# Optimization experiments

Hardware: AMD Instinct MI355X
Metric: run time of the kernel (lower is better)

Reference implementation:

```python
import jax, jax.numpy as jnp
import numpy as np
from jax import lax

N = 1000        # num_nodes
IN = 32         # in_features
H = 128         # hidden
M = 128         # message_size
DEG = 16        # regular degree
P = 2           # num_predictions
OUT = 10        # out_features
NUM_STARTS = 64


def setup_inputs() -> dict:
    key = jax.random.key(0)
    ks = jax.random.split(key, 12)
    s = 0.1
    return {
        "xa": jax.random.normal(ks[0], (N, IN), jnp.float32),
        "first_message": jax.random.normal(ks[1], (N, M), jnp.float32),
        "neighbors": jax.random.randint(ks[2], (N, DEG), 0, N, dtype=jnp.int32),
        "num_starts": NUM_STARTS,
        "enc_w": jax.random.normal(ks[3], (IN, H), jnp.float32) * s,
        "enc_b": jnp.zeros((H,), jnp.float32),
        "ns_w": jax.random.normal(ks[4], (H + M, H), jnp.float32) * s,
        "ns_b": jnp.zeros((H,), jnp.float32),
        "nm_w": jax.random.normal(ks[5], (H + M, M), jnp.float32) * s,
        "nm_b": jnp.zeros((M,), jnp.float32),
        "act_w": jax.random.normal(ks[6], (H + M, 1), jnp.float32) * s,
        "act_b": jnp.zeros((1,), jnp.float32),
        "dec_w": jax.random.normal(ks[7], (P, H, OUT), jnp.float32) * s,
        "dec_b": jnp.zeros((P, OUT), jnp.float32),
    }


def reference(xa, first_message, neighbors, num_starts,
              enc_w, enc_b, ns_w, ns_b, nm_w, nm_b, act_w, act_b, dec_w, dec_b):
    n = xa.shape[0]
    deg = neighbors.shape[1]
    m = first_message.shape[1]
    max_msgs = 10 * n                      # messages < num_nodes * 10 cap
    cap = num_starts + max_msgs * deg      # max queue size (static)

    feats0 = xa @ enc_w + enc_b            # encoder, latest state per node
    qn = jnp.zeros((cap,), jnp.int32).at[:num_starts].set(
        jnp.arange(num_starts, dtype=jnp.int32))
    qm = jnp.zeros((cap, m), feats0.dtype).at[:num_starts].set(
        first_message[:num_starts])

    carry = (jnp.int32(0), jnp.int32(num_starts), qn, qm,
             feats0, jnp.zeros_like(feats0), jnp.zeros((n,), feats0.dtype))

    def step(c, _):
        head, tail, qn, qm, feats, final, tact = c
        active = head < tail                          # queue nonempty
        node = qn[head]
        msg = lax.dynamic_slice(qm, (head, 0), (1, m))[0]
        ta = tact[node]
        proc = active & (ta <= 1.0 - 1e-7)            # ACT halting check
        f = feats[node]
        x = jnp.concatenate([f, msg])                 # [H+M]
        cand = jax.nn.sigmoid(x @ act_w + act_b)[0]
        new_act = jnp.where(ta + cand > 1.0, 1.0 - ta, cand)
        ns = jax.nn.relu(x @ ns_w + ns_b)             # new state [H]
        nm_ = jnp.concatenate([ns, msg]) @ nm_w + nm_b  # new message [M]
        # enqueue deg neighbor messages (gated write)
        old_n = lax.dynamic_slice(qn, (tail,), (deg,))
        old_m = lax.dynamic_slice(qm, (tail, 0), (deg, m))
        qn = lax.dynamic_update_slice(
            qn, jnp.where(proc, neighbors[node], old_n), (tail,))
        qm = lax.dynamic_update_slice(
            qm, jnp.where(proc, jnp.broadcast_to(nm_, (deg, m)), old_m), (tail, 0))
        feats = feats.at[node].set(jnp.where(proc, ns, f))
        final = final.at[node].add(jnp.where(proc, ns * new_act, 0.0))
        tact = tact.at[node].add(jnp.where(proc, new_act, 0.0))
        head = head + active.astype(jnp.int32)
        tail = tail + proc.astype(jnp.int32) * deg
        return (head, tail, qn, qm, feats, final, tact), None

    (_, _, _, _, _, final, _), _ = lax.scan(step, carry, None, length=max_msgs)

    g = jnp.sum(final, axis=0, keepdims=True)          # graph_class readout [1,H]
    logits = jnp.einsum('nh,pho->pno', g, dec_w) + dec_b[:, None, :]
    return jax.nn.log_softmax(logits, axis=-1)         # [P, 1, OUT]
```

## Files before the change

### kernel.cpp

```cpp
#include <hip/hip_runtime.h>
#include <math.h>

#define NN 1000
#define INF_ 32
#define H 128
#define M 128
#define DEG 16
#define PP 2
#define OUTF 10
#define MAXM (10 * NN)
#define QCAP (MAXM + DEG)
#define NSLOT (MAXM + 128)
#define NT 512
#define WQ (2 * NT)
#define WROW 264
#define NROW 136

typedef _Float16 half8 __attribute__((ext_vector_type(8)));
typedef float floatx4 __attribute__((ext_vector_type(4)));

__device__ __forceinline__ void bar_lds() {
    asm volatile("s_waitcnt lgkmcnt(0)\n\ts_barrier" ::: "memory");
}

__global__ __launch_bounds__(128)
void init_kernel(const float* __restrict__ xa, const float* __restrict__ fm,
                 const float* __restrict__ enc_w, const float* __restrict__ enc_b,
                 const int* __restrict__ nstart_p,
                 _Float16* __restrict__ feats_h, float* __restrict__ finalv,
                 _Float16* __restrict__ nmbuf_h) {
    int b = blockIdx.x, t = threadIdx.x;
    float acc = enc_b[t];
    const float* xr = xa + b * INF_;
#pragma unroll
    for (int k = 0; k < INF_; ++k) acc += xr[k] * enc_w[k * H + t];
    feats_h[b * H + t] = (_Float16)acc;
    finalv[b * H + t] = 0.0f;
    if (b < nstart_p[0]) nmbuf_h[(size_t)b * M + t] = (_Float16)fm[b * M + t];
}

__global__ __launch_bounds__(256)
void pack_kernel(const float* __restrict__ ns_w, const float* __restrict__ nm_w,
                 _Float16* __restrict__ wnsB, _Float16* __restrict__ wnmB) {
    const int idx = blockIdx.x * 256 + threadIdx.x;
    if (idx >= 128 * WROW) return;
    const int n = idx / WROW, k = idx % WROW;
    wnsB[idx] = (k < 256) ? (_Float16)ns_w[k * H + n] : (_Float16)0.0f;
    wnmB[idx] = (k < 256) ? (_Float16)nm_w[k * M + n] : (_Float16)0.0f;
}

__global__ __launch_bounds__(NT, 1)
void seq_kernel(const int* __restrict__ neighbors,
                const float* __restrict__ ns_b, const float* __restrict__ nm_b,
                const float* __restrict__ act_w, const float* __restrict__ act_b,
                const float* __restrict__ dec_w, const float* __restrict__ dec_b,
                const int* __restrict__ nstart_p,
                const _Float16* __restrict__ wnsB, const _Float16* __restrict__ wnmB,
                _Float16* __restrict__ feats_h, float* __restrict__ finalv,
                _Float16* __restrict__ nmbuf_h, unsigned int* __restrict__ qpack_unused,
                float* __restrict__ out) {
    __shared__ __align__(16) _Float16 s_Xh[2][32 * WROW];
    __shared__ __align__(16) _Float16 s_NSh[2][32 * NROW];
    __shared__ unsigned int s_q[QCAP];
    __shared__ unsigned short s_nb[NN * DEG];
    __shared__ float s_tact[NN];
    __shared__ int   s_mark[NN];
    __shared__ float s_actw[H + M];
    __shared__ float s_nsb[H];
    __shared__ float s_nmb[M];
    __shared__ float s_rna[2][32];
    __shared__ unsigned short s_rns[2 * WQ];
    __shared__ unsigned int  s_enq[WQ];
    __shared__ unsigned char s_flag[NT];
    __shared__ int s_wc[8], s_wd[8];
    __shared__ int s_cnt;

    unsigned short* const s_rnode = s_rns;
    short* s_order = (short*)s_mark;
    float* s_g  = (float*)(s_mark + 512);
    float* s_lg = (float*)(s_mark + 512 + 128);

    const int t = threadIdx.x;
    const int lane = t & 63, wid = t >> 6;
    const int quad = lane >> 4, lm = lane & 15;
    const int q4 = quad << 2;
    const int colw = (wid << 4) + lm;
    const int sg = t & 31;
    const int r16 = t >> 5, c8 = t & 31;
    const int rowc = t >> 4, c16 = t & 15;
    const int nstart = nstart_p[0];
    const int rsoff = (c8 < 16) ? 0 : WQ;
    const _Float16* const gsrc = (c8 < 16) ? (feats_h + c8 * 8)
                                           : (nmbuf_h + (c8 - 16) * 8);

    half8 wbn[8], wbm[8];
#pragma unroll
    for (int c = 0; c < 8; ++c) {
        wbn[c] = *(const half8*)(wnsB + (size_t)colw * WROW + (c << 5) + (quad << 3));
        wbm[c] = *(const half8*)(wnmB + (size_t)colw * WROW + (c << 5) + (quad << 3));
    }

    for (int i = t; i < NN; i += NT) { s_tact[i] = 0.0f; s_mark[i] = 0x7fffffff; }
    for (int i = t; i < nstart; i += NT) s_q[i] = (unsigned)i | ((unsigned)i << 16);
    for (int i = t; i < NN * DEG; i += NT) s_nb[i] = (unsigned short)neighbors[i];
    if (t < H + M) s_actw[t] = act_w[t];
    if (t < H) { s_nsb[t] = ns_b[t]; s_nmb[t] = nm_b[t]; }
    const float actb = act_b[0];
    __syncthreads();
    const float nsb_c = s_nsb[colw];
    const float nmb_c = s_nmb[colw];
    float aw[8];
#pragma unroll
    for (int j = 0; j < 8; ++j) aw[j] = s_actw[sg * 8 + j];

    auto gate = [&](uint4 v) -> float {
        const half8 hv = *(const half8*)&v;
        float p = 0.0f;
#pragma unroll
        for (int j = 0; j < 8; ++j) p += (float)hv[j] * aw[j];
#pragma unroll
        for (int off = 16; off > 0; off >>= 1) p += __shfl_down(p, off, 32);
        return p;
    };

    int head = 0, tail = nstart, gbase = nstart;
    for (;;) {
        const int lim = min(tail, MAXM);
        if (head >= lim) break;
        const int W = min(WQ, lim - head);

        int nodeA = 0, slotA = 0; bool remA = false;
        int nodeB = 0, slotB = 0; bool remB = false;
        if (t < W) {
            const unsigned v = s_q[head + t];
            nodeA = (int)(v & 0xffffu);
            slotA = (int)(v >> 16);
            remA = (s_tact[nodeA] <= 1.0f - 1e-7f);
        }
        if (NT + t < W) {
            const unsigned v = s_q[head + NT + t];
            nodeB = (int)(v & 0xffffu);
            slotB = (int)(v >> 16);
            remB = (s_tact[nodeB] <= 1.0f - 1e-7f);
        }
        s_flag[t] = 0;
        s_mark[t] = 0x7fffffff;
        bar_lds();

        int base = 0;
        for (;;) {
            const bool rem2a = remA && (s_tact[nodeA] <= 1.0f - 1e-7f);
            const bool rem2b = remB && (s_tact[nodeB] <= 1.0f - 1e-7f);
            if (rem2a) atomicMin(&s_mark[nodeA], t);
            if (rem2b) atomicMin(&s_mark[nodeB], NT + t);
            if (t == 0) s_cnt = 0;
            asm volatile("s_waitcnt vmcnt(0)" ::: "memory");
            bar_lds();
            const bool winA = rem2a && (s_mark[nodeA] == t);
            const bool winB = rem2b && (s_mark[nodeB] == NT + t);
            const unsigned long long ma = __ballot(winA);
            const unsigned long long mb = __ballot(winB);
            const int ca = __popcll(ma), cb = __popcll(mb);
            int wbase = 0;
            if (lane == 0 && (ca + cb)) wbase = atomicAdd(&s_cnt, ca + cb);
            wbase = __shfl(wbase, 0, 64);
            const unsigned long long below = (1ull << lane) - 1ull;
            if (winA) {
                const int wrank = wbase + __popcll(ma & below);
                s_rns[wrank] = (unsigned short)nodeA;
                s_rns[WQ + wrank] = (unsigned short)slotA;
                s_enq[t] = (unsigned)nodeA | ((unsigned)(gbase + base + wrank) << 16);
                s_flag[t] |= 1;
            }
            if (winB) {
                const int wrank = wbase + ca + __popcll(mb & below);
                s_rns[wrank] = (unsigned short)nodeB;
                s_rns[WQ + wrank] = (unsigned short)slotB;
                s_enq[NT + t] = (unsigned)nodeB | ((unsigned)(gbase + base + wrank) << 16);
                s_flag[t] |= 2;
            }
            remA = rem2a && !winA;
            remB = rem2b && !winB;
            bar_lds();
            if (rem2a) s_mark[nodeA] = 0x7fffffff;
            if (rem2b) s_mark[nodeB] = 0x7fffffff;
            const int Pr = s_cnt;
            if (Pr == 0) break;

            uint4 pxL = *(const uint4*)(gsrc + (size_t)s_rns[rsoff + min(r16, Pr - 1)] * 128);
            uint4 pxU = *(const uint4*)(gsrc + (size_t)s_rns[rsoff + min(16 + r16, Pr - 1)] * 128);
            *(uint4*)(s_Xh[0] + r16 * WROW + (c8 << 3)) = pxL;
            *(uint4*)(s_Xh[0] + (16 + r16) * WROW + (c8 << 3)) = pxU;
            float zredCL = gate(pxL);
            float zredCU = gate(pxU);
            if (Pr > 32) {
                pxL = *(const uint4*)(gsrc + (size_t)s_rns[rsoff + min(32 + r16, Pr - 1)] * 128);
                pxU = *(const uint4*)(gsrc + (size_t)s_rns[rsoff + min(48 + r16, Pr - 1)] * 128);
            }
            bar_lds();

            floatx4 accmPL = {0, 0, 0, 0}, accmPU = {0, 0, 0, 0};
            float nsvPL[4] = {0, 0, 0, 0}, nsvPU[4] = {0, 0, 0, 0};
            int PcPL = 0, PcPU = 0, sbP = 0, c0P = 0;

            auto phase2 = [&](int pb) {
                {
                    const _Float16* nrow = s_NSh[pb] + lm * NROW + (quad << 3);
#pragma unroll
                    for (int c = 0; c < 4; ++c)
                        accmPL = __builtin_amdgcn_mfma_f32_16x16x32_f16(
                            *(const half8*)(nrow + (c << 5)), wbm[c], accmPL, 0, 0, 0);
                }
                {
                    const _Float16* nrow = s_NSh[pb] + (16 + lm) * NROW + (quad << 3);
#pragma unroll
                    for (int c = 0; c < 4; ++c)
                        accmPU = __builtin_amdgcn_mfma_f32_16x16x32_f16(
                            *(const half8*)(nrow + (c << 5)), wbm[c], accmPU, 0, 0, 0);
                }
                float naL[4], naU[4];
                int nrL[4], nrU[4];
#pragma unroll
                for (int i = 0; i < 4; ++i) {
                    naL[i] = s_rna[pb][q4 + i];
                    naU[i] = s_rna[pb][16 + q4 + i];
                    nrL[i] = (int)s_rnode[c0P + q4 + i];
                    nrU[i] = (int)s_rnode[c0P + 16 + q4 + i];
                }
                if (PcPU == 16) {
#pragma unroll
                    for (int i = 0; i < 4; ++i) {
                        nmbuf_h[(size_t)(sbP + q4 + i) * M + colw] =
                            (_Float16)(accmPL[i] + nmb_c);
                        nmbuf_h[(size_t)(sbP + 16 + q4 + i) * M + colw] =
                            (_Float16)(accmPU[i] + nmb_c);
                    }
#pragma unroll
                    for (int i = 0; i < 4; ++i) {
                        atomicAdd(finalv + (size_t)nrL[i] * H + colw, nsvPL[i] * naL[i]);
                        atomicAdd(finalv + (size_t)nrU[i] * H + colw, nsvPU[i] * naU[i]);
                    }
                } else {
#pragma unroll
                    for (int i = 0; i < 4; ++i) {
                        const int r = q4 + i;
                        if (r < PcPL) {
                            nmbuf_h[(size_t)(sbP + r) * M + colw] =
                                (_Float16)(accmPL[i] + nmb_c);
                            atomicAdd(finalv + (size_t)nrL[i] * H + colw,
                                      nsvPL[i] * naL[i]);
                        }
                        if (r < PcPU) {
                            nmbuf_h[(size_t)(sbP + 16 + r) * M + colw] =
                                (_Float16)(accmPU[i] + nmb_c);
                            atomicAdd(finalv + (size_t)nrU[i] * H + colw,
                                      nsvPU[i] * naU[i]);
                        }
                    }
                }
                if (rowc < PcPL || (unsigned)(rowc - 16) < (unsigned)PcPU) {
                    const int nrr = (int)s_rnode[c0P + rowc];
                    const uint4 v = *(const uint4*)(s_NSh[pb] + rowc * NROW + (c16 << 3));
                    *(uint4*)(feats_h + (size_t)nrr * H + (c16 << 3)) = v;
                }
            };

            for (int c0 = 0; c0 < Pr; c0 += 32) {
                const int k = c0 >> 5;
                const int cur = k & 1, nxt = cur ^ 1;
                const int remn = Pr - c0;
                const int PcL = (remn >= 16) ? 16 : remn;
                const int PcU = (remn >= 32) ? 16 : (remn > 16 ? remn - 16 : 0);
                const bool hasnext = remn > 32;
                float zredNL = 0.0f, zredNU = 0.0f;
                if (hasnext) {
                    *(uint4*)(s_Xh[nxt] + r16 * WROW + (c8 << 3)) = pxL;
                    *(uint4*)(s_Xh[nxt] + (16 + r16) * WROW + (c8 << 3)) = pxU;
                    zredNL = gate(pxL);
                    zredNU = gate(pxU);
                }
                if (remn > 64) {
                    pxL = *(const uint4*)(gsrc + (size_t)s_rns[rsoff + min(c0 + 64 + r16, Pr - 1)] * 128);
                    pxU = *(const uint4*)(gsrc + (size_t)s_rns[rsoff + min(c0 + 80 + r16, Pr - 1)] * 128);
                }
                if (c0 > 0) phase2(nxt);
                if (sg == 0) {
                    if (r16 < PcL) {
                        const float z = zredCL + actb;
                        const float cnd = 1.0f / (1.0f + expf(-z));
                        const int nr = (int)s_rnode[c0 + r16];
                        const float ta = s_tact[nr];
                        const float na = (ta + cnd > 1.0f) ? (1.0f - ta) : cnd;
                        s_rna[cur][r16] = na;
                        s_tact[nr] = ta + na;
                    }
                    if (r16 < PcU) {
                        const float z = zredCU + actb;
                        const float cnd = 1.0f / (1.0f + expf(-z));
                        const int nr = (int)s_rnode[c0 + 16 + r16];
                        const float ta = s_tact[nr];
                        const float na = (ta + cnd > 1.0f) ? (1.0f - ta) : cnd;
                        s_rna[cur][16 + r16] = na;
                        s_tact[nr] = ta + na;
                    }
                }
                floatx4 accmL, accmU;
                float nsvL[4], nsvU[4];
                {
                    floatx4 accn = {0, 0, 0, 0}, accm = {0, 0, 0, 0};
                    const _Float16* xrow = s_Xh[cur] + lm * WROW + (quad << 3);
                    half8 a[8];
#pragma unroll
                    for (int c = 0; c < 8; ++c) a[c] = *(const half8*)(xrow + (c << 5));
#pragma unroll
                    for (int c = 0; c < 8; ++c)
                        accn = __builtin_amdgcn_mfma_f32_16x16x32_f16(a[c], wbn[c], accn, 0, 0, 0);
#pragma unroll
                    for (int c = 4; c < 8; ++c)
                        accm = __builtin_amdgcn_mfma_f32_16x16x32_f16(a[c], wbm[c], accm, 0, 0, 0);
#pragma unroll
                    for (int i = 0; i < 4; ++i) {
                        nsvL[i] = fmaxf(accn[i] + nsb_c, 0.0f);
                        s_NSh[cur][(q4 + i) * NROW + colw] = (_Float16)nsvL[i];
                    }
                    accmL = accm;
                }
                {
                    floatx4 accn = {0, 0, 0, 0}, accm = {0, 0, 0, 0};
                    const _Float16* xrow = s_Xh[cur] + (16 + lm) * WROW + (quad << 3);
                    half8 a[8];
#pragma unroll
                    for (int c = 0; c < 8; ++c) a[c] = *(const half8*)(xrow + (c << 5));
#pragma unroll
                    for (int c = 0; c < 8; ++c)
                        accn = __builtin_amdgcn_mfma_f32_16x16x32_f16(a[c], wbn[c], accn, 0, 0, 0);
#pragma unroll
                    for (int c = 4; c < 8; ++c)
                        accm = __builtin_amdgcn_mfma_f32_16x16x32_f16(a[c], wbm[c], accm, 0, 0, 0);
#pragma unroll
                    for (int i = 0; i < 4; ++i) {
                        nsvU[i] = fmaxf(accn[i] + nsb_c, 0.0f);
                        s_NSh[cur][(16 + q4 + i) * NROW + colw] = (_Float16)nsvU[i];
                    }
                    accmU = accm;
                }
                accmPL = accmL; accmPU = accmU;
#pragma unroll
                for (int i = 0; i < 4; ++i) { nsvPL[i] = nsvL[i]; nsvPU[i] = nsvU[i]; }
                PcPL = PcL; PcPU = PcU; sbP = gbase + base + c0; c0P = c0;
                zredCL = zredNL; zredCU = zredNU;
                bar_lds();
            }
            phase2((c0P >> 5) & 1);
            base += Pr;
        }

        const bool pfa = (s_flag[t] & 1) != 0;
        const bool pfb = (s_flag[t] & 2) != 0;
        const unsigned long long mfa = __ballot(pfa);
        const unsigned long long mfb = __ballot(pfb);
        if (lane == 0) { s_wc[wid] = __popcll(mfa); s_wd[wid] = __popcll(mfb); }
        bar_lds();
        int TA = 0, TB = 0, preA = 0, preB = 0;
#pragma unroll
        for (int w = 0; w < 8; ++w) {
            TA += s_wc[w]; TB += s_wd[w];
            preA += (w < wid) ? s_wc[w] : 0;
            preB += (w < wid) ? s_wd[w] : 0;
        }
        const int T = TA + TB;
        if (T > 0) {
            const unsigned long long below = (1ull << lane) - 1ull;
            if (pfa) s_order[preA + __popcll(mfa & below)] = (short)t;
            if (pfb) s_order[TA + preB + __popcll(mfb & below)] = (short)(NT + t);
            bar_lds();
            for (int idx = t; idx < T * DEG; idx += NT) {
                const int e = (int)s_order[idx >> 4];
                const unsigned v = s_enq[e];
                const int nd = (int)(v & 0xffffu);
                const unsigned slot = v >> 16;
                const int q = tail + idx;
                if (q < QCAP)
                    s_q[q] = (unsigned)s_nb[nd * DEG + (idx & 15)] | (slot << 16);
            }
        }
        tail += DEG * T;
        gbase += T;
        head += W;
        bar_lds();
    }

    __syncthreads();

    if (t < H) {
        float g0 = 0, g1 = 0, g2 = 0, g3 = 0;
        for (int n = 0; n < NN; n += 4) {
            g0 += finalv[(n + 0) * H + t];
            g1 += finalv[(n + 1) * H + t];
            g2 += finalv[(n + 2) * H + t];
            g3 += finalv[(n + 3) * H + t];
        }
        s_g[t] = (g0 + g1) + (g2 + g3);
    }
    __syncthreads();
    if (t < PP * OUTF) {
        const int pp = t / OUTF, o = t % OUTF;
        float acc = dec_b[pp * OUTF + o];
        for (int h = 0; h < H; ++h) acc += s_g[h] * dec_w[(pp * H + h) * OUTF + o];
        s_lg[t] = acc;
    }
    __syncthreads();
    if (t < PP * OUTF) {
        const int pp = t / OUTF;
        float mx = -INFINITY;
        for (int o = 0; o < OUTF; ++o) mx = fmaxf(mx, s_lg[pp * OUTF + o]);
        float s = 0.0f;
        for (int o = 0; o < OUTF; ++o) s += expf(s_lg[pp * OUTF + o] - mx);
        out[t] = s_lg[t] - (mx + logf(s));
    }
}

extern "C" void kernel_launch(void* const* d_in, const int* in_sizes, int n_in,
                              void* d_out, int out_size, void* d_ws, size_t ws_size,
                              hipStream_t stream) {
    const float* xa        = (const float*)d_in[0];
    const float* fm        = (const float*)d_in[1];
    const int*   neighbors = (const int*)  d_in[2];
    const int*   nstart_p  = (const int*)  d_in[3];
    const float* enc_w     = (const float*)d_in[4];
    const float* enc_b     = (const float*)d_in[5];
    const float* ns_w      = (const float*)d_in[6];
    const float* ns_b      = (const float*)d_in[7];
    const float* nm_w      = (const float*)d_in[8];
    const float* nm_b      = (const float*)d_in[9];
    const float* act_w     = (const float*)d_in[10];
    const float* act_b     = (const float*)d_in[11];
    const float* dec_w     = (const float*)d_in[12];
    const float* dec_b     = (const float*)d_in[13];
    float* out = (float*)d_out;

    char* w = (char*)d_ws;
    _Float16* feats_h = (_Float16*)w;                 w += (size_t)NN * H * 2;
    float*    finalv  = (float*)w;                    w += (size_t)NN * H * 4;
    _Float16* nmbuf_h = (_Float16*)w;                 w += (size_t)NSLOT * M * 2;
    _Float16* wnsB    = (_Float16*)w;                 w += (size_t)128 * WROW * 2;
    _Float16* wnmB    = (_Float16*)w;                 w += (size_t)128 * WROW * 2;
    unsigned int* qpack = (unsigned int*)w;

    init_kernel<<<NN, 128, 0, stream>>>(xa, fm, enc_w, enc_b, nstart_p,
                                        feats_h, finalv, nmbuf_h);
    pack_kernel<<<132, 256, 0, stream>>>(ns_w, nm_w, wnsB, wnmB);
    seq_kernel<<<1, NT, 0, stream>>>(neighbors, ns_b, nm_b,
                                     act_w, act_b, dec_w, dec_b, nstart_p,
                                     wnsB, wnmB,
                                     feats_h, finalv, nmbuf_h, qpack, out);
}
```

Before: 524.8 us.

## Stage new-message outputs in LDS and skip empty upper half-tiles

Inner 32-row chunks now write new-message results to an LDS staging buffer, then copy them out to global memory one iteration later as coalesced 16-byte row stores. Before, each lane did scattered 2-byte stores. The phase2 lambda is inlined and only the tail chunk keeps the guarded partial path. The upper 16-row MFMA block and its gather are skipped when a chunk has no upper rows. The vmcnt wait is moved later so it overlaps the winner-selection work. This adds LDS usage and makes the pipelining logic more complex, with a risk to correctness in edge cases.

```diff
diff --git a/kernel.cpp b/kernel.cpp
--- a/kernel.cpp
+++ b/kernel.cpp
@@ -61,6 +61,7 @@
                 float* __restrict__ out) {
     __shared__ __align__(16) _Float16 s_Xh[2][32 * WROW];
     __shared__ __align__(16) _Float16 s_NSh[2][32 * NROW];
+    __shared__ __align__(16) _Float16 s_NMh[2][32 * NROW];
     __shared__ unsigned int s_q[QCAP];
     __shared__ unsigned short s_nb[NN * DEG];
     __shared__ float s_tact[NN];
@@ -154,7 +155,6 @@
             if (rem2a) atomicMin(&s_mark[nodeA], t);
             if (rem2b) atomicMin(&s_mark[nodeB], NT + t);
             if (t == 0) s_cnt = 0;
-            asm volatile("s_waitcnt vmcnt(0)" ::: "memory");
             bar_lds();
             const bool winA = rem2a && (s_mark[nodeA] == t);
             const bool winB = rem2b && (s_mark[nodeB] == NT + t);
@@ -181,18 +181,23 @@
             }
             remA = rem2a && !winA;
             remB = rem2b && !winB;
+            asm volatile("s_waitcnt vmcnt(0)" ::: "memory");
             bar_lds();
             if (rem2a) s_mark[nodeA] = 0x7fffffff;
             if (rem2b) s_mark[nodeB] = 0x7fffffff;
             const int Pr = s_cnt;
             if (Pr == 0) break;
+            const int sb0 = gbase + base;
 
             uint4 pxL = *(const uint4*)(gsrc + (size_t)s_rns[rsoff + min(r16, Pr - 1)] * 128);
             uint4 pxU = *(const uint4*)(gsrc + (size_t)s_rns[rsoff + min(16 + r16, Pr - 1)] * 128);
             *(uint4*)(s_Xh[0] + r16 * WROW + (c8 << 3)) = pxL;
-            *(uint4*)(s_Xh[0] + (16 + r16) * WROW + (c8 << 3)) = pxU;
             float zredCL = gate(pxL);
-            float zredCU = gate(pxU);
+            float zredCU = 0.0f;
+            if (Pr > 16) {
+                *(uint4*)(s_Xh[0] + (16 + r16) * WROW + (c8 << 3)) = pxU;
+                zredCU = gate(pxU);
+            }
             if (Pr > 32) {
                 pxL = *(const uint4*)(gsrc + (size_t)s_rns[rsoff + min(32 + r16, Pr - 1)] * 128);
                 pxU = *(const uint4*)(gsrc + (size_t)s_rns[rsoff + min(48 + r16, Pr - 1)] * 128);
@@ -201,69 +206,6 @@
 
             floatx4 accmPL = {0, 0, 0, 0}, accmPU = {0, 0, 0, 0};
             float nsvPL[4] = {0, 0, 0, 0}, nsvPU[4] = {0, 0, 0, 0};
-            int PcPL = 0, PcPU = 0, sbP = 0, c0P = 0;
-
-            auto phase2 = [&](int pb) {
-                {
-                    const _Float16* nrow = s_NSh[pb] + lm * NROW + (quad << 3);
-#pragma unroll
-                    for (int c = 0; c < 4; ++c)
-                        accmPL = __builtin_amdgcn_mfma_f32_16x16x32_f16(
-                            *(const half8*)(nrow + (c << 5)), wbm[c], accmPL, 0, 0, 0);
-                }
-                {
-                    const _Float16* nrow = s_NSh[pb] + (16 + lm) * NROW + (quad << 3);
-#pragma unroll
-                    for (int c = 0; c < 4; ++c)
-                        accmPU = __builtin_amdgcn_mfma_f32_16x16x32_f16(
-                            *(const half8*)(nrow + (c << 5)), wbm[c], accmPU, 0, 0, 0);
-                }
-                float naL[4], naU[4];
-                int nrL[4], nrU[4];
-#pragma unroll
-                for (int i = 0; i < 4; ++i) {
-                    naL[i] = s_rna[pb][q4 + i];
-                    naU[i] = s_rna[pb][16 + q4 + i];
-                    nrL[i] = (int)s_rnode[c0P + q4 + i];
-                    nrU[i] = (int)s_rnode[c0P + 16 + q4 + i];
-                }
-                if (PcPU == 16) {
-#pragma unroll
-                    for (int i = 0; i < 4; ++i) {
-                        nmbuf_h[(size_t)(sbP + q4 + i) * M + colw] =
-                            (_Float16)(accmPL[i] + nmb_c);
-                        nmbuf_h[(size_t)(sbP + 16 + q4 + i) * M + colw] =
-                            (_Float16)(accmPU[i] + nmb_c);
-                    }
-#pragma unroll
-                    for (int i = 0; i < 4; ++i) {
-                        atomicAdd(finalv + (size_t)nrL[i] * H + colw, nsvPL[i] * naL[i]);
-                        atomicAdd(finalv + (size_t)nrU[i] * H + colw, nsvPU[i] * naU[i]);
-                    }
-                } else {
-#pragma unroll
-                    for (int i = 0; i < 4; ++i) {
-                        const int r = q4 + i;
-                        if (r < PcPL) {
-                            nmbuf_h[(size_t)(sbP + r) * M + colw] =
-                                (_Float16)(accmPL[i] + nmb_c);
-                            atomicAdd(finalv + (size_t)nrL[i] * H + colw,
-                                      nsvPL[i] * naL[i]);
-                        }
-                        if (r < PcPU) {
-                            nmbuf_h[(size_t)(sbP + 16 + r) * M + colw] =
-                                (_Float16)(accmPU[i] + nmb_c);
-                            atomicAdd(finalv + (size_t)nrU[i] * H + colw,
-                                      nsvPU[i] * naU[i]);
-                        }
-                    }
-                }
-                if (rowc < PcPL || (unsigned)(rowc - 16) < (unsigned)PcPU) {
-                    const int nrr = (int)s_rnode[c0P + rowc];
-                    const uint4 v = *(const uint4*)(s_NSh[pb] + rowc * NROW + (c16 << 3));
-                    *(uint4*)(feats_h + (size_t)nrr * H + (c16 << 3)) = v;
-                }
-            };
 
             for (int c0 = 0; c0 < Pr; c0 += 32) {
                 const int k = c0 >> 5;
@@ -271,19 +213,60 @@
                 const int remn = Pr - c0;
                 const int PcL = (remn >= 16) ? 16 : remn;
                 const int PcU = (remn >= 32) ? 16 : (remn > 16 ? remn - 16 : 0);
-                const bool hasnext = remn > 32;
                 float zredNL = 0.0f, zredNU = 0.0f;
-                if (hasnext) {
+                if (remn > 32) {
                     *(uint4*)(s_Xh[nxt] + r16 * WROW + (c8 << 3)) = pxL;
-                    *(uint4*)(s_Xh[nxt] + (16 + r16) * WROW + (c8 << 3)) = pxU;
                     zredNL = gate(pxL);
-                    zredNU = gate(pxU);
+                    if (remn > 48) {
+                        *(uint4*)(s_Xh[nxt] + (16 + r16) * WROW + (c8 << 3)) = pxU;
+                        zredNU = gate(pxU);
+                    }
                 }
                 if (remn > 64) {
                     pxL = *(const uint4*)(gsrc + (size_t)s_rns[rsoff + min(c0 + 64 + r16, Pr - 1)] * 128);
                     pxU = *(const uint4*)(gsrc + (size_t)s_rns[rsoff + min(c0 + 80 + r16, Pr - 1)] * 128);
                 }
-                if (c0 > 0) phase2(nxt);
+                if (c0 >= 64) {
+                    const int sbC = sb0 + c0 - 64;
+                    const uint4 v = *(const uint4*)(s_NMh[cur] + rowc * NROW + (c16 << 3));
+                    *(uint4*)(nmbuf_h + (size_t)(sbC + rowc) * M + (c16 << 3)) = v;
+                }
+                if (c0 > 0) {
+                    const int c0F = c0 - 32;
+                    {
+                        const _Float16* nrow = s_NSh[nxt] + lm * NROW + (quad << 3);
+#pragma unroll
+                        for (int c = 0; c < 4; ++c)
+                            accmPL = __builtin_amdgcn_mfma_f32_16x16x32_f16(
+                                *(const half8*)(nrow + (c << 5)), wbm[c], accmPL, 0, 0, 0);
+                    }
+                    {
+                        const _Float16* nrow = s_NSh[nxt] + (16 + lm) * NROW + (quad << 3);
+#pragma unroll
+                        for (int c = 0; c < 4; ++c)
+                            accmPU = __builtin_amdgcn_mfma_f32_16x16x32_f16(
+                                *(const half8*)(nrow + (c << 5)), wbm[c], accmPU, 0, 0, 0);
+                    }
+#pragma unroll
+                    for (int i = 0; i < 4; ++i) {
+                        s_NMh[nxt][(q4 + i) * NROW + colw] = (_Float16)(accmPL[i] + nmb_c);
+                        s_NMh[nxt][(16 + q4 + i) * NROW + colw] = (_Float16)(accmPU[i] + nmb_c);
+                    }
+#pragma unroll
+                    for (int i = 0; i < 4; ++i) {
+                        const float naL = s_rna[nxt][q4 + i];
+                        const float naU = s_rna[nxt][16 + q4 + i];
+                        const int nrL = (int)s_rnode[c0F + q4 + i];
+                        const int nrU = (int)s_rnode[c0F + 16 + q4 + i];
+                        atomicAdd(finalv + (size_t)nrL * H + colw, nsvPL[i] * naL);
+                        atomicAdd(finalv + (size_t)nrU * H + colw, nsvPU[i] * naU);
+                    }
+                    {
+                        const int nrr = (int)s_rnode[c0F + rowc];
+                        const uint4 v = *(const uint4*)(s_NSh[nxt] + rowc * NROW + (c16 << 3));
+                        *(uint4*)(feats_h + (size_t)nrr * H + (c16 << 3)) = v;
+                    }
+                }
                 if (sg == 0) {
                     if (r16 < PcL) {
                         const float z = zredCL + actb;
@@ -304,8 +287,8 @@
                         s_tact[nr] = ta + na;
                     }
                 }
-                floatx4 accmL, accmU;
-                float nsvL[4], nsvU[4];
+                floatx4 accmL = {0, 0, 0, 0}, accmU = {0, 0, 0, 0};
+                float nsvL[4] = {0, 0, 0, 0}, nsvU[4] = {0, 0, 0, 0};
                 {
                     floatx4 accn = {0, 0, 0, 0}, accm = {0, 0, 0, 0};
                     const _Float16* xrow = s_Xh[cur] + lm * WROW + (quad << 3);
@@ -325,7 +308,7 @@
                     }
                     accmL = accm;
                 }
-                {
+                if (PcU > 0) {
                     floatx4 accn = {0, 0, 0, 0}, accm = {0, 0, 0, 0};
                     const _Float16* xrow = s_Xh[cur] + (16 + lm) * WROW + (quad << 3);
                     half8 a[8];
@@ -347,11 +330,57 @@
                 accmPL = accmL; accmPU = accmU;
 #pragma unroll
                 for (int i = 0; i < 4; ++i) { nsvPL[i] = nsvL[i]; nsvPU[i] = nsvU[i]; }
-                PcPL = PcL; PcPU = PcU; sbP = gbase + base + c0; c0P = c0;
                 zredCL = zredNL; zredCU = zredNU;
                 bar_lds();
             }
-            phase2((c0P >> 5) & 1);
+            {
+                const int c0L = ((Pr - 1) >> 5) << 5;
+                const int pbL = (c0L >> 5) & 1;
+                const int lastn = Pr - c0L;
+                const int PcLL = (lastn >= 16) ? 16 : lastn;
+                const int PcLU = (lastn > 16) ? lastn - 16 : 0;
+                if (Pr > 32) {
+                    const int sbC = sb0 + c0L - 32;
+                    const uint4 v = *(const uint4*)(s_NMh[pbL ^ 1] + rowc * NROW + (c16 << 3));
+                    *(uint4*)(nmbuf_h + (size_t)(sbC + rowc) * M + (c16 << 3)) = v;
+                }
+                {
+                    const _Float16* nrow = s_NSh[pbL] + lm * NROW + (quad << 3);
+#pragma unroll
+                    for (int c = 0; c < 4; ++c)
+                        accmPL = __builtin_amdgcn_mfma_f32_16x16x32_f16(
+                            *(const half8*)(nrow + (c << 5)), wbm[c], accmPL, 0, 0, 0);
+                }
+                if (PcLU > 0) {
+                    const _Float16* nrow = s_NSh[pbL] + (16 + lm) * NROW + (quad << 3);
+#pragma unroll
+                    for (int c = 0; c < 4; ++c)
+                        accmPU = __builtin_amdgcn_mfma_f32_16x16x32_f16(
+                            *(const half8*)(nrow + (c << 5)), wbm[c], accmPU, 0, 0, 0);
+                }
+                const int sbL = sb0 + c0L;
+#pragma unroll
+                for (int i = 0; i < 4; ++i) {
+                    const int r = q4 + i;
+                    if (r < PcLL) {
+                        nmbuf_h[(size_t)(sbL + r) * M + colw] =
+                            (_Float16)(accmPL[i] + nmb_c);
+                        atomicAdd(finalv + (size_t)s_rnode[c0L + r] * H + colw,
+                                  nsvPL[i] * s_rna[pbL][r]);
+                    }
+                    if (r < PcLU) {
+                        nmbuf_h[(size_t)(sbL + 16 + r) * M + colw] =
+                            (_Float16)(accmPU[i] + nmb_c);
+                        atomicAdd(finalv + (size_t)s_rnode[c0L + 16 + r] * H + colw,
+                                  nsvPU[i] * s_rna[pbL][16 + r]);
+                    }
+                }
+                if (rowc < PcLL || (unsigned)(rowc - 16) < (unsigned)PcLU) {
+                    const int nrr = (int)s_rnode[c0L + rowc];
+                    const uint4 v = *(const uint4*)(s_NSh[pbL] + rowc * NROW + (c16 << 3));
+                    *(uint4*)(feats_h + (size_t)nrr * H + (c16 << 3)) = v;
+                }
+            }
             base += Pr;
         }
 
```

Measured after the change: 503.4 us. 1.04x faster.
